# Optimization experiments

Measured on AMD Instinct MI355X. Metric: run time of the kernel, lower is better.

The kernel has to match this reference:

```python
import jax, jax.numpy as jnp
import numpy as np

LN_EPS = 1e-5


def setup_inputs() -> dict:
    key = jax.random.key(0)
    ks = jax.random.split(key, 4)
    B, d, rank, z = 4096, 1024, 16, 1024
    hd = jax.random.normal(ks[0], (B, d), dtype=jnp.float32)
    hp = jax.random.normal(ks[1], (B, d), dtype=jnp.float32)
    U = jax.random.normal(ks[2], (rank, d, z), dtype=jnp.float32) * 0.02
    V = jax.random.normal(ks[3], (rank, d, z), dtype=jnp.float32) * 0.02
    gamma = jnp.ones((z,), dtype=jnp.float32)
    beta = jnp.zeros((z,), dtype=jnp.float32)
    return {"hd": hd, "hp": hp, "U": U, "V": V, "gamma": gamma, "beta": beta}


def reference(hd, hp, U, V, gamma, beta):
    # Low-rank Tucker bilinear fusion: sum_r (hd @ U[r]) * (hp @ V[r])
    u = jnp.einsum('bd,rdz->brz', hd, U)   # [B, rank, z]
    v = jnp.einsum('bd,rdz->brz', hp, V)   # [B, rank, z]
    z = jax.nn.relu(jnp.einsum('brz,brz->bz', u, v))  # fused mul+sum over rank
    # Dropout in eval mode = identity. LayerNorm over last dim.
    mean = jnp.mean(z, axis=-1, keepdims=True)
    var = jnp.var(z, axis=-1, keepdims=True)
    zn = (z - mean) * jax.lax.rsqrt(var + LN_EPS)
    return zn * gamma + beta
```

## Files before the change

kernel.cpp:

```cpp
#include <hip/hip_runtime.h>


typedef unsigned short u16;
typedef __attribute__((ext_vector_type(8))) short bf16x8;
typedef __attribute__((ext_vector_type(4))) float f32x4;

constexpr int Bq = 4096;
constexpr int D  = 1024;
constexpr int Zq = 1024;
constexpr int Rk = 16;

typedef const __attribute__((address_space(1))) void* gas_t;
typedef __attribute__((address_space(3))) void* las_t;

__device__ __forceinline__ u16 f2b(float f) {
  union { float f; unsigned u; } c; c.f = f;
  unsigned r = (c.u + 0x7FFFu + ((c.u >> 16) & 1u)) >> 16;
  return (u16)r;
}

__global__ __launch_bounds__(256) void fm_pack_A(const float* __restrict__ src,
                                                 u16* __restrict__ dst) {
  const int g  = blockIdx.x * 256 + threadIdx.x;
  const int c  = g & 1023;
  const int kt = (g >> 10) & 15;
  const int bx = g >> 14;
  const int l  = c & 63;
  const int kk = (c >> 6) & 1;
  const int mf = (c >> 7) & 3;
  const int wm = (c >> 9) & 1;
  const int row = wm * 64 + mf * 16 + (l & 15);
  const int kel = kk * 32 + ((l >> 4) << 3);
  const float* s = src + (size_t)(bx * 128 + row) * D + kt * 64 + kel;
  const float4 f0 = *(const float4*)s;
  const float4 f1 = *(const float4*)(s + 4);
  union { u16 h[8]; uint4 u; } o;
  o.h[0] = f2b(f0.x); o.h[1] = f2b(f0.y); o.h[2] = f2b(f0.z); o.h[3] = f2b(f0.w);
  o.h[4] = f2b(f1.x); o.h[5] = f2b(f1.y); o.h[6] = f2b(f1.z); o.h[7] = f2b(f1.w);
  *(uint4*)(dst + (size_t)g * 8) = o.u;
}

__global__ __launch_bounds__(256) void fm_pack_B(const float* __restrict__ src,
                                                 u16* __restrict__ dst) {
  const int g  = blockIdx.x * 256 + threadIdx.x;
  const int c  = g & 1023;
  const int kt = (g >> 10) & 15;
  const int jt = (g >> 14) & 7;
  const int r  = g >> 17;
  const int l  = c & 63;
  const int kk = (c >> 6) & 1;
  const int nf = (c >> 7) & 1;
  const int wn = (c >> 8) & 3;
  const int j  = jt * 128 + wn * 32 + nf * 16 + (l & 15);
  const int kg = kt * 64 + kk * 32 + ((l >> 4) << 3);
  const float* s = src + (size_t)r * (D * Zq) + (size_t)kg * Zq + j;
  union { u16 h[8]; uint4 u; } o;
  #pragma unroll
  for (int e = 0; e < 8; ++e) o.h[e] = f2b(s[(size_t)e * Zq]);
  *(uint4*)(dst + (size_t)g * 8) = o.u;
}

#define STAGE(buf, ktile) do {                                                   \
    const int _o = (ktile) * 8192;                                               \
    __builtin_amdgcn_global_load_lds((gas_t)(hdp + _o + c0 * 8), (las_t)&sT[buf][0][c0 * 8], 16, 0, 0); \
    __builtin_amdgcn_global_load_lds((gas_t)(hdp + _o + c1 * 8), (las_t)&sT[buf][0][c1 * 8], 16, 0, 0); \
    __builtin_amdgcn_global_load_lds((gas_t)(hpp + _o + c0 * 8), (las_t)&sT[buf][1][c0 * 8], 16, 0, 0); \
    __builtin_amdgcn_global_load_lds((gas_t)(hpp + _o + c1 * 8), (las_t)&sT[buf][1][c1 * 8], 16, 0, 0); \
  } while (0)

#define LOADB(BU, BV, stp) do {                                                  \
    const u16* _up = Ub + (size_t)((stp) >> 4) * rstride + ((stp) & 15) * 8192;  \
    const u16* _vp = Vb + (size_t)((stp) >> 4) * rstride + ((stp) & 15) * 8192;  \
    _Pragma("unroll")                                                            \
    for (int nf = 0; nf < 2; ++nf)                                               \
      _Pragma("unroll")                                                          \
      for (int kk = 0; kk < 2; ++kk) {                                           \
        BU[nf][kk] = *(const bf16x8*)(_up + bco[nf][kk]);                        \
        BV[nf][kk] = *(const bf16x8*)(_vp + bco[nf][kk]);                        \
      }                                                                          \
  } while (0)

#define COMPUTE(buf, BU, BV) do {                                                \
    const u16* tA = sT[buf][0];                                                  \
    const u16* tB = sT[buf][1];                                                  \
    _Pragma("unroll")                                                            \
    for (int kk = 0; kk < 2; ++kk) {                                             \
      bf16x8 a[4], b[4];                                                         \
      _Pragma("unroll")                                                          \
      for (int mf = 0; mf < 4; ++mf) {                                           \
        const int ao = (((wm * 4 + mf) * 2 + kk) * 64 + lane) * 8;               \
        a[mf] = *(const bf16x8*)(tA + ao);                                       \
        b[mf] = *(const bf16x8*)(tB + ao);                                       \
      }                                                                          \
      __builtin_amdgcn_s_setprio(1);                                             \
      _Pragma("unroll")                                                          \
      for (int mf = 0; mf < 4; ++mf)                                             \
        _Pragma("unroll")                                                        \
        for (int nf = 0; nf < 2; ++nf) {                                         \
          au[mf][nf] = __builtin_amdgcn_mfma_f32_16x16x32_bf16(a[mf], BU[nf][kk], au[mf][nf], 0, 0, 0); \
          av[mf][nf] = __builtin_amdgcn_mfma_f32_16x16x32_bf16(b[mf], BV[nf][kk], av[mf][nf], 0, 0, 0); \
        }                                                                        \
      __builtin_amdgcn_s_setprio(0);                                             \
    }                                                                            \
  } while (0)

#define SFENCE() __builtin_amdgcn_sched_barrier(0)
#define BAR()    __builtin_amdgcn_s_barrier()

#define PHASE(buf, BU, BV, s) do {                                               \
    COMPUTE(buf, BU, BV);                                                        \
    BAR(); SFENCE();                                                             \
    if ((s) + 2 < 256) {                                                         \
      STAGE(buf, ((s) + 2) & 15);                                                \
      LOADB(BU, BV, (s) + 2);                                                    \
      SFENCE();                                                                  \
      asm volatile("s_waitcnt vmcnt(12)" ::: "memory");                          \
    } else {                                                                     \
      asm volatile("s_waitcnt vmcnt(0)" ::: "memory");                           \
    }                                                                            \
    SFENCE();                                                                    \
    BAR(); SFENCE();                                                             \
  } while (0)

__global__ __launch_bounds__(512, 2) void fused_bilinear(
    const u16* __restrict__ hdf, const u16* __restrict__ hpf,
    const u16* __restrict__ Uf, const u16* __restrict__ Vf,
    float* __restrict__ out)
{
  __shared__ __align__(16) u16 sT[2][2][128 * 64];

  const int tid  = threadIdx.x;
  const int lane = tid & 63;
  const int wv   = tid >> 6;
  const int wm   = wv >> 2;
  const int wn   = wv & 3;

  const int bx = blockIdx.x;
  const int jt = blockIdx.y;

  const u16* hdp = hdf + (size_t)bx * 16 * 8192;
  const u16* hpp = hpf + (size_t)bx * 16 * 8192;
  const u16* Ub  = Uf + (size_t)jt * 16 * 8192;
  const u16* Vb  = Vf + (size_t)jt * 16 * 8192;
  const size_t rstride = (size_t)8 * 16 * 8192;

  const int c0 = wv * 128 + lane;
  const int c1 = c0 + 64;

  int bco[2][2];
  #pragma unroll
  for (int nf = 0; nf < 2; ++nf)
    #pragma unroll
    for (int kk = 0; kk < 2; ++kk)
      bco[nf][kk] = (((wn * 2 + nf) * 2 + kk) * 64 + lane) * 8;

  f32x4 acc[4][2], au[4][2], av[4][2];
  #pragma unroll
  for (int mf = 0; mf < 4; ++mf)
    #pragma unroll
    for (int nf = 0; nf < 2; ++nf) {
      acc[mf][nf] = (f32x4){0.f, 0.f, 0.f, 0.f};
      au[mf][nf]  = (f32x4){0.f, 0.f, 0.f, 0.f};
      av[mf][nf]  = (f32x4){0.f, 0.f, 0.f, 0.f};
    }

  bf16x8 bu0[2][2], bv0[2][2], bu1[2][2], bv1[2][2];

  STAGE(0, 0); LOADB(bu0, bv0, 0);
  STAGE(1, 1); LOADB(bu1, bv1, 1);
  SFENCE();
  asm volatile("s_waitcnt vmcnt(12)" ::: "memory");
  SFENCE();
  BAR(); SFENCE();

  #pragma unroll 1
  for (int it = 0; it < 128; ++it) {
    const int s0 = it * 2;
    const int s1 = s0 + 1;

    PHASE(0, bu0, bv0, s0);
    PHASE(1, bu1, bv1, s1);

    if ((s1 & 15) == 15) {
      #pragma unroll
      for (int mf = 0; mf < 4; ++mf)
        #pragma unroll
        for (int nf = 0; nf < 2; ++nf) {
          #pragma unroll
          for (int i = 0; i < 4; ++i)
            acc[mf][nf][i] += au[mf][nf][i] * av[mf][nf][i];
          au[mf][nf] = (f32x4){0.f, 0.f, 0.f, 0.f};
          av[mf][nf] = (f32x4){0.f, 0.f, 0.f, 0.f};
        }
    }
  }

  const int brow = bx * 128;
  const int jcol = jt * 128;
  #pragma unroll
  for (int mf = 0; mf < 4; ++mf)
    #pragma unroll
    for (int nf = 0; nf < 2; ++nf) {
      const int gr = brow + wm * 64 + mf * 16 + ((lane >> 4) << 2);
      const int gc = jcol + wn * 32 + nf * 16 + (lane & 15);
      #pragma unroll
      for (int i = 0; i < 4; ++i)
        out[(size_t)(gr + i) * Zq + gc] = acc[mf][nf][i];
    }
}

__global__ __launch_bounds__(256) void ln_rows(float* __restrict__ out,
    const float* __restrict__ gamma, const float* __restrict__ beta)
{
  const int row = blockIdx.x;
  const int t = threadIdx.x;
  float* o = out + (size_t)row * Zq;
  float4 v = ((const float4*)o)[t];
  v.x = fmaxf(v.x, 0.f); v.y = fmaxf(v.y, 0.f);
  v.z = fmaxf(v.z, 0.f); v.w = fmaxf(v.w, 0.f);
  float s = v.x + v.y + v.z + v.w;
  float q = v.x * v.x + v.y * v.y + v.z * v.z + v.w * v.w;
  #pragma unroll
  for (int off = 32; off > 0; off >>= 1) {
    s += __shfl_xor(s, off);
    q += __shfl_xor(q, off);
  }
  __shared__ float ss[4], sq[4];
  if ((t & 63) == 0) { ss[t >> 6] = s; sq[t >> 6] = q; }
  __syncthreads();
  s = ss[0] + ss[1] + ss[2] + ss[3];
  q = sq[0] + sq[1] + sq[2] + sq[3];
  const float mean = s * (1.f / Zq);
  float var = q * (1.f / Zq) - mean * mean;
  var = fmaxf(var, 0.f);
  const float rstd = rsqrtf(var + 1e-5f);
  const float4 g  = ((const float4*)gamma)[t];
  const float4 bb = ((const float4*)beta)[t];
  v.x = (v.x - mean) * rstd * g.x + bb.x;
  v.y = (v.y - mean) * rstd * g.y + bb.y;
  v.z = (v.z - mean) * rstd * g.z + bb.z;
  v.w = (v.w - mean) * rstd * g.w + bb.w;
  ((float4*)o)[t] = v;
}

__global__ __launch_bounds__(256) void fallback_bilinear(
    const float* __restrict__ hd, const float* __restrict__ hp,
    const float* __restrict__ U, const float* __restrict__ V,
    float* __restrict__ out)
{
  const int j  = blockIdx.x * 256 + threadIdx.x;
  const int b0 = blockIdx.y * 8;
  float acc[8] = {0.f, 0.f, 0.f, 0.f, 0.f, 0.f, 0.f, 0.f};
  for (int r = 0; r < Rk; ++r) {
    float u[8] = {0.f}, v[8] = {0.f};
    const float* Up = U + (size_t)r * (D * Zq) + j;
    const float* Vp = V + (size_t)r * (D * Zq) + j;
    for (int k = 0; k < D; ++k) {
      const float uu = Up[(size_t)k * Zq];
      const float vv = Vp[(size_t)k * Zq];
      #pragma unroll
      for (int bi = 0; bi < 8; ++bi) {
        u[bi] = fmaf(hd[(size_t)(b0 + bi) * D + k], uu, u[bi]);
        v[bi] = fmaf(hp[(size_t)(b0 + bi) * D + k], vv, v[bi]);
      }
    }
    #pragma unroll
    for (int bi = 0; bi < 8; ++bi) acc[bi] += u[bi] * v[bi];
  }
  #pragma unroll
  for (int bi = 0; bi < 8; ++bi)
    out[(size_t)(b0 + bi) * Zq + j] = acc[bi];
}

extern "C" void kernel_launch(void* const* d_in, const int* in_sizes, int n_in,
                              void* d_out, int out_size, void* d_ws, size_t ws_size,
                              hipStream_t stream) {
  const float* hd    = (const float*)d_in[0];
  const float* hp    = (const float*)d_in[1];
  const float* U     = (const float*)d_in[2];
  const float* V     = (const float*)d_in[3];
  const float* gamma = (const float*)d_in[4];
  const float* beta  = (const float*)d_in[5];
  float* out = (float*)d_out;

  const size_t need = 80ull << 20;
  if (ws_size >= need) {
    u16* hdf = (u16*)d_ws;
    u16* hpf = hdf + (size_t)Bq * D;
    u16* Ufm = hpf + (size_t)Bq * D;
    u16* Vfm = Ufm + (size_t)Rk * D * Zq;

    fm_pack_A<<<2048, 256, 0, stream>>>(hd, hdf);
    fm_pack_A<<<2048, 256, 0, stream>>>(hp, hpf);
    fm_pack_B<<<8192, 256, 0, stream>>>(U, Ufm);
    fm_pack_B<<<8192, 256, 0, stream>>>(V, Vfm);
    fused_bilinear<<<dim3(32, 8), 512, 0, stream>>>(hdf, hpf, Ufm, Vfm, out);
  } else {
    fallback_bilinear<<<dim3(Zq / 256, Bq / 8), 256, 0, stream>>>(hd, hp, U, V, out);
  }
  ln_rows<<<Bq, 256, 0, stream>>>(out, gamma, beta);
}
```

Measured before the change: 419.8 us.

## Interleave B-fragment prefetch and LDS staging across four sub-phases per k-step

Replaces the two-phase compute/stage structure with a four-sub-phase step. Each sub-phase loads two A/B fragments from LDS and issues eight MFMAs, and the global loads for the next step's U/V fragments are spread across sub-phases. This halves the register-held B fragment buffers, one set instead of two double-buffered sets, which may cut register pressure, and it spreads memory traffic between MFMA bursts. The cost is more barriers per step, plus B loads now have only one sub-phase of latency slack, which risks exposed global-load latency.

```diff
diff --git a/kernel.cpp b/kernel.cpp
--- a/kernel.cpp
+++ b/kernel.cpp
@@ -60,67 +60,74 @@
   *(uint4*)(dst + (size_t)g * 8) = o.u;
 }
 
-#define STAGE(buf, ktile) do {                                                   \
-    const int _o = (ktile) * 8192;                                               \
-    __builtin_amdgcn_global_load_lds((gas_t)(hdp + _o + c0 * 8), (las_t)&sT[buf][0][c0 * 8], 16, 0, 0); \
-    __builtin_amdgcn_global_load_lds((gas_t)(hdp + _o + c1 * 8), (las_t)&sT[buf][0][c1 * 8], 16, 0, 0); \
-    __builtin_amdgcn_global_load_lds((gas_t)(hpp + _o + c0 * 8), (las_t)&sT[buf][1][c0 * 8], 16, 0, 0); \
-    __builtin_amdgcn_global_load_lds((gas_t)(hpp + _o + c1 * 8), (las_t)&sT[buf][1][c1 * 8], 16, 0, 0); \
-  } while (0)
-
-#define LOADB(BU, BV, stp) do {                                                  \
-    const u16* _up = Ub + (size_t)((stp) >> 4) * rstride + ((stp) & 15) * 8192;  \
-    const u16* _vp = Vb + (size_t)((stp) >> 4) * rstride + ((stp) & 15) * 8192;  \
-    _Pragma("unroll")                                                            \
-    for (int nf = 0; nf < 2; ++nf)                                               \
-      _Pragma("unroll")                                                          \
-      for (int kk = 0; kk < 2; ++kk) {                                           \
-        BU[nf][kk] = *(const bf16x8*)(_up + bco[nf][kk]);                        \
-        BV[nf][kk] = *(const bf16x8*)(_vp + bco[nf][kk]);                        \
-      }                                                                          \
-  } while (0)
-
-#define COMPUTE(buf, BU, BV) do {                                                \
-    const u16* tA = sT[buf][0];                                                  \
-    const u16* tB = sT[buf][1];                                                  \
-    _Pragma("unroll")                                                            \
-    for (int kk = 0; kk < 2; ++kk) {                                             \
-      bf16x8 a[4], b[4];                                                         \
-      _Pragma("unroll")                                                          \
-      for (int mf = 0; mf < 4; ++mf) {                                           \
-        const int ao = (((wm * 4 + mf) * 2 + kk) * 64 + lane) * 8;               \
-        a[mf] = *(const bf16x8*)(tA + ao);                                       \
-        b[mf] = *(const bf16x8*)(tB + ao);                                       \
-      }                                                                          \
-      __builtin_amdgcn_s_setprio(1);                                             \
-      _Pragma("unroll")                                                          \
-      for (int mf = 0; mf < 4; ++mf)                                             \
-        _Pragma("unroll")                                                        \
-        for (int nf = 0; nf < 2; ++nf) {                                         \
-          au[mf][nf] = __builtin_amdgcn_mfma_f32_16x16x32_bf16(a[mf], BU[nf][kk], au[mf][nf], 0, 0, 0); \
-          av[mf][nf] = __builtin_amdgcn_mfma_f32_16x16x32_bf16(b[mf], BV[nf][kk], av[mf][nf], 0, 0, 0); \
-        }                                                                        \
-      __builtin_amdgcn_s_setprio(0);                                             \
-    }                                                                            \
-  } while (0)
-
+#define GLDS(src, dst) __builtin_amdgcn_global_load_lds((gas_t)(src), (las_t)(dst), 16, 0, 0)
 #define SFENCE() __builtin_amdgcn_sched_barrier(0)
 #define BAR()    __builtin_amdgcn_s_barrier()
-
-#define PHASE(buf, BU, BV, s) do {                                               \
-    COMPUTE(buf, BU, BV);                                                        \
-    BAR(); SFENCE();                                                             \
-    if ((s) + 2 < 256) {                                                         \
-      STAGE(buf, ((s) + 2) & 15);                                                \
-      LOADB(BU, BV, (s) + 2);                                                    \
-      SFENCE();                                                                  \
-      asm volatile("s_waitcnt vmcnt(12)" ::: "memory");                          \
-    } else {                                                                     \
-      asm volatile("s_waitcnt vmcnt(0)" ::: "memory");                           \
+#define MFMA __builtin_amdgcn_mfma_f32_16x16x32_bf16
+
+#define STEP(buf, s) do {                                                        \
+  const u16* tA = sT[buf][0];                                                    \
+  const u16* tB = sT[buf][1];                                                    \
+  const bool pf1 = (s) + 1 < 256;                                                \
+  const bool pf2 = (s) + 2 < 256;                                                \
+  const int kn2 = ((s) + 2) & 15;                                                \
+  const u16* upn = Ub + (size_t)(((s)+1) >> 4) * rstride + (((s)+1) & 15) * 8192;\
+  const u16* vpn = Vb + (size_t)(((s)+1) >> 4) * rstride + (((s)+1) & 15) * 8192;\
+  _Pragma("unroll")                                                              \
+  for (int p = 0; p < 4; ++p) {                                                  \
+    const int kk = p >> 1, mh = (p & 1) << 1;                                    \
+    const int r0 = (((wm * 4 + mh) * 2 + kk) * 64 + lane) * 8;                   \
+    bf16x8 a0 = *(const bf16x8*)(tA + r0);                                       \
+    bf16x8 a1 = *(const bf16x8*)(tA + r0 + 1024);                                \
+    bf16x8 b0 = *(const bf16x8*)(tB + r0);                                       \
+    bf16x8 b1 = *(const bf16x8*)(tB + r0 + 1024);                                \
+    if (p == 2 && pf1) {          \
+      bu[0][0] = *(const bf16x8*)(upn + bco[0][0]);                              \
+      bu[1][0] = *(const bf16x8*)(upn + bco[1][0]);                              \
+      bv[0][0] = *(const bf16x8*)(vpn + bco[0][0]);                              \
+      bv[1][0] = *(const bf16x8*)(vpn + bco[1][0]);                              \
     }                                                                            \
     SFENCE();                                                                    \
-    BAR(); SFENCE();                                                             \
-  } while (0)
+    BAR();                                                                       \
+    asm volatile("s_waitcnt lgkmcnt(0)" ::: "memory");                           \
+    SFENCE();                                                                    \
+    __builtin_amdgcn_s_setprio(1);                                               \
+    au[mh][0]     = MFMA(a0, bu[0][kk], au[mh][0], 0, 0, 0);                     \
+    av[mh][0]     = MFMA(b0, bv[0][kk], av[mh][0], 0, 0, 0);                     \
+    au[mh][1]     = MFMA(a0, bu[1][kk], au[mh][1], 0, 0, 0);                     \
+    av[mh][1]     = MFMA(b0, bv[1][kk], av[mh][1], 0, 0, 0);                     \
+    au[mh + 1][0] = MFMA(a1, bu[0][kk], au[mh + 1][0], 0, 0, 0);                 \
+    av[mh + 1][0] = MFMA(b1, bv[0][kk], av[mh + 1][0], 0, 0, 0);                 \
+    au[mh + 1][1] = MFMA(a1, bu[1][kk], au[mh + 1][1], 0, 0, 0);                 \
+    av[mh + 1][1] = MFMA(b1, bv[1][kk], av[mh + 1][1], 0, 0, 0);                 \
+    __builtin_amdgcn_s_setprio(0);                                               \
+    if (p == 3) {                                                                \
+      if (pf1) {                            \
+        bu[0][1] = *(const bf16x8*)(upn + bco[0][1]);                            \
+        bu[1][1] = *(const bf16x8*)(upn + bco[1][1]);                            \
+        bv[0][1] = *(const bf16x8*)(vpn + bco[0][1]);                            \
+        bv[1][1] = *(const bf16x8*)(vpn + bco[1][1]);                            \
+      }                                                                          \
+      if (pf2) {                 \
+        GLDS(hdp + kn2 * 8192 + c0 * 8, &sT[buf][0][c0 * 8]);                    \
+        GLDS(hdp + kn2 * 8192 + c1 * 8, &sT[buf][0][c1 * 8]);                    \
+        GLDS(hpp + kn2 * 8192 + c0 * 8, &sT[buf][1][c0 * 8]);                    \
+        GLDS(hpp + kn2 * 8192 + c1 * 8, &sT[buf][1][c1 * 8]);                    \
+        SFENCE();                                                                \
+        asm volatile("s_waitcnt vmcnt(12)" ::: "memory");                        \
+      } else if ((s) == 254) {                                                   \
+        SFENCE();                                                                \
+        asm volatile("s_waitcnt vmcnt(8)" ::: "memory");                         \
+      } else {                                                                   \
+        SFENCE();                                                                \
+        asm volatile("s_waitcnt vmcnt(0)" ::: "memory");                         \
+      }                                                                          \
+    }                                                                            \
+    SFENCE();                                                                    \
+    BAR();                                                                       \
+    SFENCE();                                                                    \
+  }                                                                              \
+} while (0)
 
 __global__ __launch_bounds__(512, 2) void fused_bilinear(
     const u16* __restrict__ hdf, const u16* __restrict__ hpf,
@@ -164,12 +171,25 @@
       av[mf][nf]  = (f32x4){0.f, 0.f, 0.f, 0.f};
     }
 
-  bf16x8 bu0[2][2], bv0[2][2], bu1[2][2], bv1[2][2];
-
-  STAGE(0, 0); LOADB(bu0, bv0, 0);
-  STAGE(1, 1); LOADB(bu1, bv1, 1);
+  bf16x8 bu[2][2], bv[2][2];
+
+  GLDS(hdp + 0 * 8192 + c0 * 8, &sT[0][0][c0 * 8]);
+  GLDS(hdp + 0 * 8192 + c1 * 8, &sT[0][0][c1 * 8]);
+  GLDS(hpp + 0 * 8192 + c0 * 8, &sT[0][1][c0 * 8]);
+  GLDS(hpp + 0 * 8192 + c1 * 8, &sT[0][1][c1 * 8]);
+  GLDS(hdp + 1 * 8192 + c0 * 8, &sT[1][0][c0 * 8]);
+  GLDS(hdp + 1 * 8192 + c1 * 8, &sT[1][0][c1 * 8]);
+  GLDS(hpp + 1 * 8192 + c0 * 8, &sT[1][1][c0 * 8]);
+  GLDS(hpp + 1 * 8192 + c1 * 8, &sT[1][1][c1 * 8]);
+  #pragma unroll
+  for (int nf = 0; nf < 2; ++nf)
+    #pragma unroll
+    for (int kk = 0; kk < 2; ++kk) {
+      bu[nf][kk] = *(const bf16x8*)(Ub + bco[nf][kk]);
+      bv[nf][kk] = *(const bf16x8*)(Vb + bco[nf][kk]);
+    }
   SFENCE();
-  asm volatile("s_waitcnt vmcnt(12)" ::: "memory");
+  asm volatile("s_waitcnt vmcnt(0)" ::: "memory");
   SFENCE();
   BAR(); SFENCE();
 
@@ -178,8 +198,8 @@
     const int s0 = it * 2;
     const int s1 = s0 + 1;
 
-    PHASE(0, bu0, bv0, s0);
-    PHASE(1, bu1, bv1, s1);
+    STEP(0, s0);
+    STEP(1, s1);
 
     if ((s1 & 15) == 15) {
       #pragma unroll
```

After: 414.9 us. Within noise of the previous version (-1.2%).
